# Optimization experiments

Hardware: AMD Instinct MI355X
Metric: run time of the kernel (lower is better)

## Reference

```python
import jax, jax.numpy as jnp
import numpy as np

N = 50000      # atoms
E = 800000     # edges (avg degree 32)
H = 64         # hidden_channels
F = 64         # num_filters
G = 50         # num_gaussians
L = 6          # num_interactions
B = 128        # graphs in batch
MAX_Z = 100
CUTOFF = 10.0


def setup_inputs() -> dict:
    key = jax.random.key(0)
    ks = jax.random.split(key, 20)
    s = 0.05  # weight scale
    return {
        "z": jax.random.randint(ks[0], (N,), 0, MAX_Z, dtype=jnp.int32),
        "pos": jax.random.uniform(ks[1], (N, 3), dtype=jnp.float32) * 5.0,
        "batch": jnp.sort(jax.random.randint(ks[2], (N,), 0, B, dtype=jnp.int32)),
        "edge_index": jax.random.randint(ks[3], (2, E), 0, N, dtype=jnp.int32),
        "embed": jax.random.normal(ks[4], (MAX_Z, H), dtype=jnp.float32) * s,
        "mlp_w1": jax.random.normal(ks[5], (L, G, F), dtype=jnp.float32) * s,
        "mlp_b1": jax.random.normal(ks[6], (L, F), dtype=jnp.float32) * s,
        "mlp_w2": jax.random.normal(ks[7], (L, F, F), dtype=jnp.float32) * s,
        "mlp_b2": jax.random.normal(ks[8], (L, F), dtype=jnp.float32) * s,
        "lin_w": jax.random.normal(ks[9], (L, H, F), dtype=jnp.float32) * s,
        "lin_out_w": jax.random.normal(ks[10], (L, F, H), dtype=jnp.float32) * s,
        "lin_out_b": jax.random.normal(ks[11], (L, H), dtype=jnp.float32) * s,
        "fc1_w": jax.random.normal(ks[12], (H, H // 2), dtype=jnp.float32) * s,
        "fc1_b": jax.random.normal(ks[13], (H // 2,), dtype=jnp.float32) * s,
        "fc2_w": jax.random.normal(ks[14], (H // 2, 1), dtype=jnp.float32) * s,
        "fc2_b": jax.random.normal(ks[15], (1,), dtype=jnp.float32) * s,
    }


def reference(z, pos, batch, edge_index, embed, mlp_w1, mlp_b1, mlp_w2, mlp_b2,
              lin_w, lin_out_w, lin_out_b, fc1_w, fc1_b, fc2_w, fc2_b):
    src, dst = edge_index[0], edge_index[1]
    # edge distances (replaces the python cdist loop; edge list is precomputed)
    d = jnp.sqrt(jnp.sum((pos[src] - pos[dst]) ** 2, axis=-1))  # [E]
    # Gaussian smearing
    offset = jnp.linspace(0.0, CUTOFF, G)
    coeff = -0.5 / (offset[1] - offset[0]) ** 2
    edge_attr = jnp.exp(coeff * (d[:, None] - offset) ** 2)  # [E, G]
    # cosine cutoff
    cut = 0.5 * (jnp.cos(d * np.pi / CUTOFF) + 1.0) * (d < CUTOFF).astype(d.dtype)  # [E]

    h = embed[z]  # [N, H]
    for l in range(L):
        # filter MLP on edge features, modulated by cutoff
        W = jnp.tanh(edge_attr @ mlp_w1[l] + mlp_b1[l]) @ mlp_w2[l] + mlp_b2[l]  # [E, F]
        W = W * cut[:, None]
        h_j = h @ lin_w[l]  # [N, F]
        messages = h_j[src] * W  # gather + modulate  [E, F]
        agg = jax.ops.segment_sum(messages, dst, num_segments=N)  # scatter-add [N, F]
        h = h + (agg @ lin_out_w[l] + lin_out_b[l])  # residual

    # global mean pool over graphs
    sums = jax.ops.segment_sum(h, batch, num_segments=B)  # [B, H]
    cnt = jax.ops.segment_sum(jnp.ones((h.shape[0],), h.dtype), batch, num_segments=B)
    pooled = sums / jnp.maximum(cnt, 1.0)[:, None]

    x = jax.nn.relu(pooled @ fc1_w + fc1_b)  # dropout = identity (eval)
    return x @ fc2_w + fc2_b  # [B, 1]
```

## Files before the change

### kernel.cpp

```cpp
#include <hip/hip_runtime.h>
#include <math.h>

#define E_EDGES 800000
#define N_ATOMS 50000
#define N_GRAPH 128
#define P_TBL   4096
#define SCAN_NB 49

static constexpr float PI_F   = 3.14159265358979323846f;
static constexpr float GSTEP  = 10.0f / 49.0f;
static constexpr float GCOEFF = -0.5f / (GSTEP * GSTEP);
static constexpr float DMAX   = 8.6603f;
static constexpr float DSCALE = (float)(P_TBL - 1) / DMAX;

__global__ void hist_kernel(const int* __restrict__ dst, int* __restrict__ cnt) {
    int e = blockIdx.x * 256 + threadIdx.x;
    if (e < E_EDGES) atomicAdd(&cnt[dst[e]], 1);
}

__global__ __launch_bounds__(1024)
void scan1_kernel(const int* __restrict__ cnt, int* __restrict__ local_ex,
                  int* __restrict__ bsum) {
    __shared__ int sh[1024];
    const int t = threadIdx.x;
    const int i = blockIdx.x * 1024 + t;
    const int v = (i < N_ATOMS) ? cnt[i] : 0;
    sh[t] = v;
    __syncthreads();
    #pragma unroll
    for (int off = 1; off < 1024; off <<= 1) {
        int u = (t >= off) ? sh[t - off] : 0;
        __syncthreads();
        sh[t] += u;
        __syncthreads();
    }
    if (i < N_ATOMS) local_ex[i] = sh[t] - v;
    if (t == 1023) bsum[blockIdx.x] = sh[t];
}

__global__ __launch_bounds__(1024)
void scan2_kernel(const int* __restrict__ local_ex, const int* __restrict__ bsum,
                  int* __restrict__ starts, int* __restrict__ cursor) {
    __shared__ int off;
    const int b = blockIdx.x;
    if (threadIdx.x < 64) {
        int v = (threadIdx.x < b) ? bsum[threadIdx.x] : 0;
        #pragma unroll
        for (int d = 32; d > 0; d >>= 1) v += __shfl_down(v, d, 64);
        if (threadIdx.x == 0) off = v;
    }
    __syncthreads();
    const int i = b * 1024 + threadIdx.x;
    if (i < N_ATOMS) {
        int v = local_ex[i] + off;
        starts[i] = v;
        cursor[i] = v;
    }
}

__global__ void scatter_kernel(const int* __restrict__ ei, const float* __restrict__ pos,
                               int* __restrict__ cursor, uint2* __restrict__ pk) {
    int e = blockIdx.x * 256 + threadIdx.x;
    if (e >= E_EDGES) return;
    int sidx = ei[e];
    int dd   = ei[E_EDGES + e];
    float dx = pos[3*sidx+0] - pos[3*dd+0];
    float dy = pos[3*sidx+1] - pos[3*dd+1];
    float dz = pos[3*sidx+2] - pos[3*dd+2];
    float dist = sqrtf(dx*dx + dy*dy + dz*dz);
    int p = atomicAdd(&cursor[dd], 1);
    pk[p] = make_uint2((unsigned)sidx, __float_as_uint(dist));
}

__global__ __launch_bounds__(256)
void table_kernel(const float* __restrict__ w1, const float* __restrict__ b1,
                  const float* __restrict__ w2, const float* __restrict__ b2,
                  float* __restrict__ tbl) {
    __shared__ float sa[4][52];
    __shared__ float st[4][64];
    const int l  = blockIdx.x >> 10;
    const int rb = blockIdx.x & 1023;
    const int rr = threadIdx.x >> 6;
    const int f  = threadIdx.x & 63;
    const int r  = rb * 4 + rr;
    const float dp = (float)r * (DMAX / (float)(P_TBL - 1));

    if (f < 50) {
        float t = dp - (float)f * GSTEP;
        sa[rr][f] = expf(GCOEFF * t * t);
    }
    __syncthreads();

    const float* W1 = w1 + (size_t)l * 50 * 64;
    const float* W2 = w2 + (size_t)l * 64 * 64;
    float t = b1[l * 64 + f];
    #pragma unroll 5
    for (int g = 0; g < 50; ++g) t = fmaf(sa[rr][g], W1[g * 64 + f], t);
    st[rr][f] = tanhf(t);
    __syncthreads();

    float w = b2[l * 64 + f];
    #pragma unroll 8
    for (int k = 0; k < 64; ++k) w = fmaf(st[rr][k], W2[k * 64 + f], w);
    float cutv = 0.5f * (cosf(dp * (PI_F / 10.0f)) + 1.0f);
    tbl[((size_t)l * P_TBL + r) * 64 + f] = w * cutv;
}

__global__ __launch_bounds__(256)
void embed_lin0_kernel(const int* __restrict__ z, const float* __restrict__ embed,
                       const float* __restrict__ W,
                       float* __restrict__ h, float* __restrict__ hj) {
    __shared__ float sA[64 * 65];
    __shared__ float sW[64 * 64];
    const int tid = threadIdx.x;
    const int rbase = blockIdx.x * 64;

    for (int i = tid; i < 64 * 64; i += 256) sW[i] = W[i];
    for (int i = tid; i < 64 * 64; i += 256) {
        int r = i >> 6, k = i & 63;
        int row = rbase + r;
        float v = 0.0f;
        if (row < N_ATOMS) {
            v = embed[(size_t)z[row] * 64 + k];
            h[(size_t)row * 64 + k] = v;
        }
        sA[r * 65 + k] = v;
    }
    __syncthreads();

    const int f0 = (tid & 7) * 8;
    const int r0 = (tid >> 3) * 2;
    float acc[2][8];
    #pragma unroll
    for (int i = 0; i < 2; ++i)
        #pragma unroll
        for (int j = 0; j < 8; ++j) acc[i][j] = 0.0f;

    #pragma unroll 4
    for (int k = 0; k < 64; ++k) {
        float a[2] = { sA[(r0+0)*65 + k], sA[(r0+1)*65 + k] };
        float4 wa = *(const float4*)&sW[k * 64 + f0];
        float4 wb = *(const float4*)&sW[k * 64 + f0 + 4];
        float w[8] = {wa.x, wa.y, wa.z, wa.w, wb.x, wb.y, wb.z, wb.w};
        #pragma unroll
        for (int i = 0; i < 2; ++i)
            #pragma unroll
            for (int j = 0; j < 8; ++j)
                acc[i][j] = fmaf(a[i], w[j], acc[i][j]);
    }

    #pragma unroll
    for (int i = 0; i < 2; ++i) {
        int row = rbase + r0 + i;
        if (row < N_ATOMS) {
            float* o = hj + (size_t)row * 64;
            *(float4*)&o[f0]     = make_float4(acc[i][0], acc[i][1], acc[i][2], acc[i][3]);
            *(float4*)&o[f0 + 4] = make_float4(acc[i][4], acc[i][5], acc[i][6], acc[i][7]);
        }
    }
}

__device__ __forceinline__ float edge_w(const float* __restrict__ tbl, float dist, int f) {
    float x = dist * DSCALE;
    int i0 = (int)x; i0 = (i0 > P_TBL - 2) ? (P_TBL - 2) : i0;
    float fr = x - (float)i0;
    float t0 = tbl[i0 * 64 + f];
    float t1 = tbl[i0 * 64 + 64 + f];
    return fmaf(fr, t1 - t0, t0);
}

__global__ __launch_bounds__(256)
void layer_kernel(const uint2* __restrict__ pk,
                  const int* __restrict__ starts, const int* __restrict__ cnts,
                  const float* __restrict__ hj_in, const float* __restrict__ tbl,
                  const float* __restrict__ Wout, const float* __restrict__ bout,
                  float* __restrict__ h,
                  const float* __restrict__ Wlin, float* __restrict__ hj_out,
                  int doLin) {
    __shared__ float sA[64 * 65];
    __shared__ float sW[64 * 64];
    __shared__ float sb[64];
    const int tid = threadIdx.x;
    const int rbase = blockIdx.x * 64;
    const int f  = tid & 63;
    const int wv = tid >> 6;

    for (int i = tid; i < 64 * 64; i += 256) sW[i] = Wout[i];
    if (tid < 64) sb[tid] = bout[tid];

    for (int i = 0; i < 16; ++i) {
        const int r = wv * 16 + i;
        const int n = rbase + r;
        float res = 0.0f;
        if (n < N_ATOMS) {
            const int s   = starts[n];
            const int end = s + cnts[n];
            float a0 = 0.0f, a1 = 0.0f, a2 = 0.0f, a3 = 0.0f;
            float a4 = 0.0f, a5 = 0.0f, a6 = 0.0f, a7 = 0.0f;
            int e = s;
            for (; e + 8 <= end; e += 8) {
                uint2 p0 = pk[e+0], p1 = pk[e+1], p2 = pk[e+2], p3 = pk[e+3];
                uint2 p4 = pk[e+4], p5 = pk[e+5], p6 = pk[e+6], p7 = pk[e+7];
                float w0 = edge_w(tbl, __uint_as_float(p0.y), f);
                float w1 = edge_w(tbl, __uint_as_float(p1.y), f);
                float w2 = edge_w(tbl, __uint_as_float(p2.y), f);
                float w3 = edge_w(tbl, __uint_as_float(p3.y), f);
                float w4 = edge_w(tbl, __uint_as_float(p4.y), f);
                float w5 = edge_w(tbl, __uint_as_float(p5.y), f);
                float w6 = edge_w(tbl, __uint_as_float(p6.y), f);
                float w7 = edge_w(tbl, __uint_as_float(p7.y), f);
                a0 = fmaf(w0, hj_in[(size_t)p0.x * 64 + f], a0);
                a1 = fmaf(w1, hj_in[(size_t)p1.x * 64 + f], a1);
                a2 = fmaf(w2, hj_in[(size_t)p2.x * 64 + f], a2);
                a3 = fmaf(w3, hj_in[(size_t)p3.x * 64 + f], a3);
                a4 = fmaf(w4, hj_in[(size_t)p4.x * 64 + f], a4);
                a5 = fmaf(w5, hj_in[(size_t)p5.x * 64 + f], a5);
                a6 = fmaf(w6, hj_in[(size_t)p6.x * 64 + f], a6);
                a7 = fmaf(w7, hj_in[(size_t)p7.x * 64 + f], a7);
            }
            for (; e + 2 <= end; e += 2) {
                uint2 p0 = pk[e], p1 = pk[e+1];
                float w0 = edge_w(tbl, __uint_as_float(p0.y), f);
                float w1 = edge_w(tbl, __uint_as_float(p1.y), f);
                a0 = fmaf(w0, hj_in[(size_t)p0.x * 64 + f], a0);
                a1 = fmaf(w1, hj_in[(size_t)p1.x * 64 + f], a1);
            }
            if (e < end) {
                uint2 p0 = pk[e];
                float w0 = edge_w(tbl, __uint_as_float(p0.y), f);
                a0 = fmaf(w0, hj_in[(size_t)p0.x * 64 + f], a0);
            }
            res = ((a0 + a1) + (a2 + a3)) + ((a4 + a5) + (a6 + a7));
        }
        sA[r * 65 + f] = res;
    }
    __syncthreads();

    const int f0 = (tid & 7) * 8;
    const int r0 = (tid >> 3) * 2;

    float acc[2][8];
    #pragma unroll
    for (int i = 0; i < 2; ++i) {
        int row = rbase + r0 + i;
        if (row < N_ATOMS) {
            const float* hr = h + (size_t)row * 64;
            float4 h0 = *(const float4*)&hr[f0];
            float4 h1 = *(const float4*)&hr[f0 + 4];
            acc[i][0] = h0.x + sb[f0+0]; acc[i][1] = h0.y + sb[f0+1];
            acc[i][2] = h0.z + sb[f0+2]; acc[i][3] = h0.w + sb[f0+3];
            acc[i][4] = h1.x + sb[f0+4]; acc[i][5] = h1.y + sb[f0+5];
            acc[i][6] = h1.z + sb[f0+6]; acc[i][7] = h1.w + sb[f0+7];
        } else {
            #pragma unroll
            for (int j = 0; j < 8; ++j) acc[i][j] = 0.0f;
        }
    }

    #pragma unroll 4
    for (int k = 0; k < 64; ++k) {
        float a[2] = { sA[(r0+0)*65 + k], sA[(r0+1)*65 + k] };
        float4 wa = *(const float4*)&sW[k * 64 + f0];
        float4 wb = *(const float4*)&sW[k * 64 + f0 + 4];
        float w[8] = {wa.x, wa.y, wa.z, wa.w, wb.x, wb.y, wb.z, wb.w};
        #pragma unroll
        for (int i = 0; i < 2; ++i)
            #pragma unroll
            for (int j = 0; j < 8; ++j)
                acc[i][j] = fmaf(a[i], w[j], acc[i][j]);
    }
    __syncthreads();

    #pragma unroll
    for (int i = 0; i < 2; ++i) {
        int row = rbase + r0 + i;
        if (row < N_ATOMS) {
            float* o = h + (size_t)row * 64;
            *(float4*)&o[f0]     = make_float4(acc[i][0], acc[i][1], acc[i][2], acc[i][3]);
            *(float4*)&o[f0 + 4] = make_float4(acc[i][4], acc[i][5], acc[i][6], acc[i][7]);
        }
        #pragma unroll
        for (int j = 0; j < 8; ++j)
            sA[(r0 + i) * 65 + f0 + j] = acc[i][j];
    }
    if (!doLin) return;
    for (int i = tid; i < 64 * 64; i += 256) sW[i] = Wlin[i];
    __syncthreads();

    float acc2[2][8];
    #pragma unroll
    for (int i = 0; i < 2; ++i)
        #pragma unroll
        for (int j = 0; j < 8; ++j) acc2[i][j] = 0.0f;

    #pragma unroll 4
    for (int k = 0; k < 64; ++k) {
        float a[2] = { sA[(r0+0)*65 + k], sA[(r0+1)*65 + k] };
        float4 wa = *(const float4*)&sW[k * 64 + f0];
        float4 wb = *(const float4*)&sW[k * 64 + f0 + 4];
        float w[8] = {wa.x, wa.y, wa.z, wa.w, wb.x, wb.y, wb.z, wb.w};
        #pragma unroll
        for (int i = 0; i < 2; ++i)
            #pragma unroll
            for (int j = 0; j < 8; ++j)
                acc2[i][j] = fmaf(a[i], w[j], acc2[i][j]);
    }

    #pragma unroll
    for (int i = 0; i < 2; ++i) {
        int row = rbase + r0 + i;
        if (row < N_ATOMS) {
            float* o = hj_out + (size_t)row * 64;
            *(float4*)&o[f0]     = make_float4(acc2[i][0], acc2[i][1], acc2[i][2], acc2[i][3]);
            *(float4*)&o[f0 + 4] = make_float4(acc2[i][4], acc2[i][5], acc2[i][6], acc2[i][7]);
        }
    }
}

__global__ __launch_bounds__(256)
void pool_head_kernel(const float* __restrict__ h, const int* __restrict__ batch,
                      const float* __restrict__ fc1w, const float* __restrict__ fc1b,
                      const float* __restrict__ fc2w, const float* __restrict__ fc2b,
                      float* __restrict__ out) {
    __shared__ float part[4][64];
    __shared__ float sp[64];
    __shared__ float sx[32];
    __shared__ int bounds[2];
    const int g   = blockIdx.x;
    const int tid = threadIdx.x;

    if (tid < 2) {
        int target = g + tid;
        int lo = 0, hi = N_ATOMS;
        while (lo < hi) {
            int m = (lo + hi) >> 1;
            if (batch[m] < target) lo = m + 1; else hi = m;
        }
        bounds[tid] = lo;
    }
    __syncthreads();
    const int s = bounds[0], epos = bounds[1];

    const int f = tid & 63, wv = tid >> 6;
    float a = 0.0f;
    for (int r = s + wv; r < epos; r += 4) a += h[(size_t)r * 64 + f];
    part[wv][f] = a;
    __syncthreads();

    if (tid < 64) {
        float cnt = (float)(epos - s);
        sp[tid] = (part[0][tid] + part[1][tid] + part[2][tid] + part[3][tid])
                  / fmaxf(cnt, 1.0f);
    }
    __syncthreads();
    if (tid < 32) {
        float a1 = fc1b[tid];
        #pragma unroll 8
        for (int k = 0; k < 64; ++k) a1 = fmaf(sp[k], fc1w[k * 32 + tid], a1);
        sx[tid] = fmaxf(a1, 0.0f);
    }
    __syncthreads();
    if (tid == 0) {
        float a2 = fc2b[0];
        #pragma unroll 8
        for (int j = 0; j < 32; ++j) a2 = fmaf(sx[j], fc2w[j], a2);
        out[g] = a2;
    }
}

extern "C" void kernel_launch(void* const* d_in, const int* in_sizes, int n_in,
                              void* d_out, int out_size, void* d_ws, size_t ws_size,
                              hipStream_t stream) {
    const int*   z         = (const int*)  d_in[0];
    const float* pos       = (const float*)d_in[1];
    const int*   batch     = (const int*)  d_in[2];
    const int*   ei        = (const int*)  d_in[3];
    const float* embed     = (const float*)d_in[4];
    const float* mlp_w1    = (const float*)d_in[5];
    const float* mlp_b1    = (const float*)d_in[6];
    const float* mlp_w2    = (const float*)d_in[7];
    const float* mlp_b2    = (const float*)d_in[8];
    const float* lin_w     = (const float*)d_in[9];
    const float* lin_out_w = (const float*)d_in[10];
    const float* lin_out_b = (const float*)d_in[11];
    const float* fc1w      = (const float*)d_in[12];
    const float* fc1b      = (const float*)d_in[13];
    const float* fc2w      = (const float*)d_in[14];
    const float* fc2b      = (const float*)d_in[15];
    float* out = (float*)d_out;

    float* ws    = (float*)d_ws;
    float* h     = ws;
    float* hj0   = h     + (size_t)N_ATOMS * 64;
    float* hj1   = hj0   + (size_t)N_ATOMS * 64;
    float* tbl   = hj1   + (size_t)N_ATOMS * 64;
    uint2* pk    = (uint2*)(tbl + (size_t)6 * P_TBL * 64);
    int*   hist  = (int*)(pk + E_EDGES);
    int*   starts= hist  + N_ATOMS;
    int*   cursor= starts+ N_ATOMS;
    int*   lex   = cursor+ N_ATOMS;
    int*   bsum  = lex   + N_ATOMS;

    const int* dst = ei + E_EDGES;

    hipMemsetAsync(hist, 0, N_ATOMS * sizeof(int), stream);
    hist_kernel<<<E_EDGES / 256, 256, 0, stream>>>(dst, hist);
    scan1_kernel<<<SCAN_NB, 1024, 0, stream>>>(hist, lex, bsum);
    scan2_kernel<<<SCAN_NB, 1024, 0, stream>>>(lex, bsum, starts, cursor);
    scatter_kernel<<<E_EDGES / 256, 256, 0, stream>>>(ei, pos, cursor, pk);
    table_kernel<<<6 * (P_TBL / 4), 256, 0, stream>>>(mlp_w1, mlp_b1, mlp_w2, mlp_b2, tbl);

    const int ngemm_grid = (N_ATOMS + 63) / 64;

    embed_lin0_kernel<<<ngemm_grid, 256, 0, stream>>>(z, embed, lin_w, h, hj0);

    float* hjbuf[2] = { hj0, hj1 };
    for (int l = 0; l < 6; ++l) {
        layer_kernel<<<ngemm_grid, 256, 0, stream>>>(
            pk, starts, hist, hjbuf[l & 1], tbl + (size_t)l * P_TBL * 64,
            lin_out_w + (size_t)l * 64 * 64, lin_out_b + (size_t)l * 64, h,
            (l < 5) ? (lin_w + (size_t)(l + 1) * 64 * 64) : nullptr,
            hjbuf[(l + 1) & 1], (l < 5) ? 1 : 0);
    }

    pool_head_kernel<<<N_GRAPH, 256, 0, stream>>>(h, batch, fc1w, fc1b, fc2w, fc2b, out);
}
```

Before: 717.4 us.

## Interleave interpolation table pairs and restructure layer kernel to wave-local rows

The filter table is stored as interleaved (t[i], t[i+1]) float2 pairs, so each edge weight interpolation needs one 8-byte load instead of two scalar loads. The layer kernel now runs 512 threads per block, with each wave owning 8 atom rows through both the gather and the two 64x64 GEMMs. Block-wide barriers between phases become wave barriers, and Wout and Wlin are both staged into shared memory up front. The risks are a doubled table footprint and higher shared memory per block (two weight tiles), which may reduce occupancy.

```diff
diff --git a/kernel.cpp b/kernel.cpp
--- a/kernel.cpp
+++ b/kernel.cpp
@@ -75,7 +75,7 @@
 __global__ __launch_bounds__(256)
 void table_kernel(const float* __restrict__ w1, const float* __restrict__ b1,
                   const float* __restrict__ w2, const float* __restrict__ b2,
-                  float* __restrict__ tbl) {
+                  float* __restrict__ tbl2) {
     __shared__ float sa[4][52];
     __shared__ float st[4][64];
     const int l  = blockIdx.x >> 10;
@@ -103,7 +103,10 @@
     #pragma unroll 8
     for (int k = 0; k < 64; ++k) w = fmaf(st[rr][k], W2[k * 64 + f], w);
     float cutv = 0.5f * (cosf(dp * (PI_F / 10.0f)) + 1.0f);
-    tbl[((size_t)l * P_TBL + r) * 64 + f] = w * cutv;
+    float val = w * cutv;
+    const size_t base = ((size_t)l * P_TBL + r) * 64 + f;
+    tbl2[base * 2 + 0] = val;
+    if (r > 0) tbl2[(base - 64) * 2 + 1] = val;
 }
 
 __global__ __launch_bounds__(256)
@@ -160,36 +163,49 @@
     }
 }
 
-__device__ __forceinline__ float edge_w(const float* __restrict__ tbl, float dist, int f) {
+__device__ __forceinline__ float edge_w2(const float2* __restrict__ tbl, float dist, int f) {
     float x = dist * DSCALE;
     int i0 = (int)x; i0 = (i0 > P_TBL - 2) ? (P_TBL - 2) : i0;
     float fr = x - (float)i0;
-    float t0 = tbl[i0 * 64 + f];
-    float t1 = tbl[i0 * 64 + 64 + f];
-    return fmaf(fr, t1 - t0, t0);
-}
-
-__global__ __launch_bounds__(256)
+    float2 t = tbl[i0 * 64 + f];
+    return fmaf(fr, t.y - t.x, t.x);
+}
+
+__global__ __launch_bounds__(512)
 void layer_kernel(const uint2* __restrict__ pk,
                   const int* __restrict__ starts, const int* __restrict__ cnts,
-                  const float* __restrict__ hj_in, const float* __restrict__ tbl,
+                  const float* __restrict__ hj_in, const float2* __restrict__ tbl,
                   const float* __restrict__ Wout, const float* __restrict__ bout,
                   float* __restrict__ h,
                   const float* __restrict__ Wlin, float* __restrict__ hj_out,
                   int doLin) {
     __shared__ float sA[64 * 65];
-    __shared__ float sW[64 * 64];
+    __shared__ float sW1[64 * 64];
+    __shared__ float sW2[64 * 64];
     __shared__ float sb[64];
     const int tid = threadIdx.x;
     const int rbase = blockIdx.x * 64;
     const int f  = tid & 63;
     const int wv = tid >> 6;
-
-    for (int i = tid; i < 64 * 64; i += 256) sW[i] = Wout[i];
+    const int r0 = tid >> 3;
+    const int f0 = (tid & 7) * 8;
+    const int myrow = rbase + r0;
+
+    float4 hA = make_float4(0.f,0.f,0.f,0.f), hB = hA;
+    if (myrow < N_ATOMS) {
+        const float* hr = h + (size_t)myrow * 64;
+        hA = *(const float4*)&hr[f0];
+        hB = *(const float4*)&hr[f0 + 4];
+    }
+
+    for (int i = tid; i < 64 * 64; i += 512) sW1[i] = Wout[i];
+    if (doLin)
+        for (int i = tid; i < 64 * 64; i += 512) sW2[i] = Wlin[i];
     if (tid < 64) sb[tid] = bout[tid];
-
-    for (int i = 0; i < 16; ++i) {
-        const int r = wv * 16 + i;
+    __syncthreads();
+
+    for (int i = 0; i < 8; ++i) {
+        const int r = wv * 8 + i;
         const int n = rbase + r;
         float res = 0.0f;
         if (n < N_ATOMS) {
@@ -201,14 +217,14 @@
             for (; e + 8 <= end; e += 8) {
                 uint2 p0 = pk[e+0], p1 = pk[e+1], p2 = pk[e+2], p3 = pk[e+3];
                 uint2 p4 = pk[e+4], p5 = pk[e+5], p6 = pk[e+6], p7 = pk[e+7];
-                float w0 = edge_w(tbl, __uint_as_float(p0.y), f);
-                float w1 = edge_w(tbl, __uint_as_float(p1.y), f);
-                float w2 = edge_w(tbl, __uint_as_float(p2.y), f);
-                float w3 = edge_w(tbl, __uint_as_float(p3.y), f);
-                float w4 = edge_w(tbl, __uint_as_float(p4.y), f);
-                float w5 = edge_w(tbl, __uint_as_float(p5.y), f);
-                float w6 = edge_w(tbl, __uint_as_float(p6.y), f);
-                float w7 = edge_w(tbl, __uint_as_float(p7.y), f);
+                float w0 = edge_w2(tbl, __uint_as_float(p0.y), f);
+                float w1 = edge_w2(tbl, __uint_as_float(p1.y), f);
+                float w2 = edge_w2(tbl, __uint_as_float(p2.y), f);
+                float w3 = edge_w2(tbl, __uint_as_float(p3.y), f);
+                float w4 = edge_w2(tbl, __uint_as_float(p4.y), f);
+                float w5 = edge_w2(tbl, __uint_as_float(p5.y), f);
+                float w6 = edge_w2(tbl, __uint_as_float(p6.y), f);
+                float w7 = edge_w2(tbl, __uint_as_float(p7.y), f);
                 a0 = fmaf(w0, hj_in[(size_t)p0.x * 64 + f], a0);
                 a1 = fmaf(w1, hj_in[(size_t)p1.x * 64 + f], a1);
                 a2 = fmaf(w2, hj_in[(size_t)p2.x * 64 + f], a2);
@@ -220,100 +236,69 @@
             }
             for (; e + 2 <= end; e += 2) {
                 uint2 p0 = pk[e], p1 = pk[e+1];
-                float w0 = edge_w(tbl, __uint_as_float(p0.y), f);
-                float w1 = edge_w(tbl, __uint_as_float(p1.y), f);
+                float w0 = edge_w2(tbl, __uint_as_float(p0.y), f);
+                float w1 = edge_w2(tbl, __uint_as_float(p1.y), f);
                 a0 = fmaf(w0, hj_in[(size_t)p0.x * 64 + f], a0);
                 a1 = fmaf(w1, hj_in[(size_t)p1.x * 64 + f], a1);
             }
             if (e < end) {
                 uint2 p0 = pk[e];
-                float w0 = edge_w(tbl, __uint_as_float(p0.y), f);
+                float w0 = edge_w2(tbl, __uint_as_float(p0.y), f);
                 a0 = fmaf(w0, hj_in[(size_t)p0.x * 64 + f], a0);
             }
             res = ((a0 + a1) + (a2 + a3)) + ((a4 + a5) + (a6 + a7));
         }
         sA[r * 65 + f] = res;
     }
-    __syncthreads();
-
-    const int f0 = (tid & 7) * 8;
-    const int r0 = (tid >> 3) * 2;
-
-    float acc[2][8];
-    #pragma unroll
-    for (int i = 0; i < 2; ++i) {
-        int row = rbase + r0 + i;
-        if (row < N_ATOMS) {
-            const float* hr = h + (size_t)row * 64;
-            float4 h0 = *(const float4*)&hr[f0];
-            float4 h1 = *(const float4*)&hr[f0 + 4];
-            acc[i][0] = h0.x + sb[f0+0]; acc[i][1] = h0.y + sb[f0+1];
-            acc[i][2] = h0.z + sb[f0+2]; acc[i][3] = h0.w + sb[f0+3];
-            acc[i][4] = h1.x + sb[f0+4]; acc[i][5] = h1.y + sb[f0+5];
-            acc[i][6] = h1.z + sb[f0+6]; acc[i][7] = h1.w + sb[f0+7];
-        } else {
-            #pragma unroll
-            for (int j = 0; j < 8; ++j) acc[i][j] = 0.0f;
-        }
-    }
+    __builtin_amdgcn_wave_barrier();
+
+    float acc[8];
+    acc[0] = hA.x + sb[f0+0]; acc[1] = hA.y + sb[f0+1];
+    acc[2] = hA.z + sb[f0+2]; acc[3] = hA.w + sb[f0+3];
+    acc[4] = hB.x + sb[f0+4]; acc[5] = hB.y + sb[f0+5];
+    acc[6] = hB.z + sb[f0+6]; acc[7] = hB.w + sb[f0+7];
 
     #pragma unroll 4
     for (int k = 0; k < 64; ++k) {
-        float a[2] = { sA[(r0+0)*65 + k], sA[(r0+1)*65 + k] };
-        float4 wa = *(const float4*)&sW[k * 64 + f0];
-        float4 wb = *(const float4*)&sW[k * 64 + f0 + 4];
-        float w[8] = {wa.x, wa.y, wa.z, wa.w, wb.x, wb.y, wb.z, wb.w};
-        #pragma unroll
-        for (int i = 0; i < 2; ++i)
-            #pragma unroll
-            for (int j = 0; j < 8; ++j)
-                acc[i][j] = fmaf(a[i], w[j], acc[i][j]);
-    }
-    __syncthreads();
-
+        float a = sA[r0 * 65 + k];
+        float4 wa = *(const float4*)&sW1[k * 64 + f0];
+        float4 wb = *(const float4*)&sW1[k * 64 + f0 + 4];
+        acc[0] = fmaf(a, wa.x, acc[0]); acc[1] = fmaf(a, wa.y, acc[1]);
+        acc[2] = fmaf(a, wa.z, acc[2]); acc[3] = fmaf(a, wa.w, acc[3]);
+        acc[4] = fmaf(a, wb.x, acc[4]); acc[5] = fmaf(a, wb.y, acc[5]);
+        acc[6] = fmaf(a, wb.z, acc[6]); acc[7] = fmaf(a, wb.w, acc[7]);
+    }
+    __builtin_amdgcn_wave_barrier();
+
+    if (myrow < N_ATOMS) {
+        float* o = h + (size_t)myrow * 64;
+        *(float4*)&o[f0]     = make_float4(acc[0], acc[1], acc[2], acc[3]);
+        *(float4*)&o[f0 + 4] = make_float4(acc[4], acc[5], acc[6], acc[7]);
+    }
     #pragma unroll
-    for (int i = 0; i < 2; ++i) {
-        int row = rbase + r0 + i;
-        if (row < N_ATOMS) {
-            float* o = h + (size_t)row * 64;
-            *(float4*)&o[f0]     = make_float4(acc[i][0], acc[i][1], acc[i][2], acc[i][3]);
-            *(float4*)&o[f0 + 4] = make_float4(acc[i][4], acc[i][5], acc[i][6], acc[i][7]);
-        }
-        #pragma unroll
-        for (int j = 0; j < 8; ++j)
-            sA[(r0 + i) * 65 + f0 + j] = acc[i][j];
-    }
+    for (int j = 0; j < 8; ++j) sA[r0 * 65 + f0 + j] = acc[j];
     if (!doLin) return;
-    for (int i = tid; i < 64 * 64; i += 256) sW[i] = Wlin[i];
-    __syncthreads();
-
-    float acc2[2][8];
+    __builtin_amdgcn_wave_barrier();
+
+    float acc2[8];
     #pragma unroll
-    for (int i = 0; i < 2; ++i)
-        #pragma unroll
-        for (int j = 0; j < 8; ++j) acc2[i][j] = 0.0f;
+    for (int j = 0; j < 8; ++j) acc2[j] = 0.0f;
 
     #pragma unroll 4
     for (int k = 0; k < 64; ++k) {
-        float a[2] = { sA[(r0+0)*65 + k], sA[(r0+1)*65 + k] };
-        float4 wa = *(const float4*)&sW[k * 64 + f0];
-        float4 wb = *(const float4*)&sW[k * 64 + f0 + 4];
-        float w[8] = {wa.x, wa.y, wa.z, wa.w, wb.x, wb.y, wb.z, wb.w};
-        #pragma unroll
-        for (int i = 0; i < 2; ++i)
-            #pragma unroll
-            for (int j = 0; j < 8; ++j)
-                acc2[i][j] = fmaf(a[i], w[j], acc2[i][j]);
-    }
-
-    #pragma unroll
-    for (int i = 0; i < 2; ++i) {
-        int row = rbase + r0 + i;
-        if (row < N_ATOMS) {
-            float* o = hj_out + (size_t)row * 64;
-            *(float4*)&o[f0]     = make_float4(acc2[i][0], acc2[i][1], acc2[i][2], acc2[i][3]);
-            *(float4*)&o[f0 + 4] = make_float4(acc2[i][4], acc2[i][5], acc2[i][6], acc2[i][7]);
-        }
+        float a = sA[r0 * 65 + k];
+        float4 wa = *(const float4*)&sW2[k * 64 + f0];
+        float4 wb = *(const float4*)&sW2[k * 64 + f0 + 4];
+        acc2[0] = fmaf(a, wa.x, acc2[0]); acc2[1] = fmaf(a, wa.y, acc2[1]);
+        acc2[2] = fmaf(a, wa.z, acc2[2]); acc2[3] = fmaf(a, wa.w, acc2[3]);
+        acc2[4] = fmaf(a, wb.x, acc2[4]); acc2[5] = fmaf(a, wb.y, acc2[5]);
+        acc2[6] = fmaf(a, wb.z, acc2[6]); acc2[7] = fmaf(a, wb.w, acc2[7]);
+    }
+
+    if (myrow < N_ATOMS) {
+        float* o = hj_out + (size_t)myrow * 64;
+        *(float4*)&o[f0]     = make_float4(acc2[0], acc2[1], acc2[2], acc2[3]);
+        *(float4*)&o[f0 + 4] = make_float4(acc2[4], acc2[5], acc2[6], acc2[7]);
     }
 }
 
@@ -389,17 +374,17 @@
     const float* fc2b      = (const float*)d_in[15];
     float* out = (float*)d_out;
 
-    float* ws    = (float*)d_ws;
-    float* h     = ws;
-    float* hj0   = h     + (size_t)N_ATOMS * 64;
-    float* hj1   = hj0   + (size_t)N_ATOMS * 64;
-    float* tbl   = hj1   + (size_t)N_ATOMS * 64;
-    uint2* pk    = (uint2*)(tbl + (size_t)6 * P_TBL * 64);
-    int*   hist  = (int*)(pk + E_EDGES);
-    int*   starts= hist  + N_ATOMS;
-    int*   cursor= starts+ N_ATOMS;
-    int*   lex   = cursor+ N_ATOMS;
-    int*   bsum  = lex   + N_ATOMS;
+    float*  ws    = (float*)d_ws;
+    float*  h     = ws;
+    float*  hj0   = h     + (size_t)N_ATOMS * 64;
+    float*  hj1   = hj0   + (size_t)N_ATOMS * 64;
+    float2* tbl   = (float2*)(hj1 + (size_t)N_ATOMS * 64);
+    uint2*  pk    = (uint2*)(tbl + (size_t)6 * P_TBL * 64);
+    int*    hist  = (int*)(pk + E_EDGES);
+    int*    starts= hist  + N_ATOMS;
+    int*    cursor= starts+ N_ATOMS;
+    int*    lex   = cursor+ N_ATOMS;
+    int*    bsum  = lex   + N_ATOMS;
 
     const int* dst = ei + E_EDGES;
 
@@ -408,7 +393,8 @@
     scan1_kernel<<<SCAN_NB, 1024, 0, stream>>>(hist, lex, bsum);
     scan2_kernel<<<SCAN_NB, 1024, 0, stream>>>(lex, bsum, starts, cursor);
     scatter_kernel<<<E_EDGES / 256, 256, 0, stream>>>(ei, pos, cursor, pk);
-    table_kernel<<<6 * (P_TBL / 4), 256, 0, stream>>>(mlp_w1, mlp_b1, mlp_w2, mlp_b2, tbl);
+    table_kernel<<<6 * (P_TBL / 4), 256, 0, stream>>>(mlp_w1, mlp_b1, mlp_w2, mlp_b2,
+                                                      (float*)tbl);
 
     const int ngemm_grid = (N_ATOMS + 63) / 64;
 
@@ -416,7 +402,7 @@
 
     float* hjbuf[2] = { hj0, hj1 };
     for (int l = 0; l < 6; ++l) {
-        layer_kernel<<<ngemm_grid, 256, 0, stream>>>(
+        layer_kernel<<<ngemm_grid, 512, 0, stream>>>(
             pk, starts, hist, hjbuf[l & 1], tbl + (size_t)l * P_TBL * 64,
             lin_out_w + (size_t)l * 64 * 64, lin_out_b + (size_t)l * 64, h,
             (l < 5) ? (lin_w + (size_t)(l + 1) * 64 * 64) : nullptr,
```

Result: no change. 729.4 us (+1.7%).
